# Kernel optimization log

Measured on AMD Instinct MI355X. Metric: run time of the kernel, lower is better.

## Reference

```python
import jax, jax.numpy as jnp
import numpy as np

N = 8192
E = 131072
IN_DIM = 3000
HID = 512      # gcn1 out = HID // 2 = 256
OUT = 64
EPS = 1e-12


def gcn_conv(x, W, b, src, dst, n):
    """PyG GCNConv: add self-loops, symmetric norm, gather-matmul-scatter."""
    xw = x @ W                                   # [n, out]
    loop = jnp.arange(n, dtype=src.dtype)
    s = jnp.concatenate([src, loop])             # source j
    d = jnp.concatenate([dst, loop])             # target i
    deg = jax.ops.segment_sum(jnp.ones(s.shape[0], dtype=xw.dtype), d, num_segments=n)
    dinv = deg ** -0.5                           # deg >= 1 due to self-loops
    norm = dinv[s] * dinv[d]                     # [E+n]
    out = jax.ops.segment_sum(norm[:, None] * xw[s], d, num_segments=n)
    return out + b


def avg_readout(emb, mask):
    vsum = mask @ emb                            # [N, h]
    row_sum = jnp.sum(mask, axis=1, keepdims=True)
    g = vsum / row_sum
    nrm = jnp.maximum(jnp.linalg.norm(g, axis=1, keepdims=True), EPS)
    return g / nrm                               # F.normalize(p=2, dim=1)


def bilinear(h, c, Wd, bd):
    # nn.Bilinear(n_h, n_h, 1): out[n,o] = sum_ij h[n,i] Wd[o,i,j] c[n,j] + bd[o]
    return jnp.einsum('ni,oij,nj->no', h, Wd, c) + bd


def setup_inputs() -> dict:
    key = jax.random.key(0)
    k1, k2, k3, k4, k5, k6, k7 = jax.random.split(key, 7)
    gene_data = jax.random.normal(k1, (N, IN_DIM), dtype=jnp.float32)
    # sparse binary neighborhood mask (~16 neighbors/row) + self so row sums > 0
    mask = (jax.random.uniform(k2, (N, N)) < (16.0 / N)).astype(jnp.float32)
    mask = jnp.maximum(mask, jnp.eye(N, dtype=jnp.float32))
    spatial_edge_index = jax.random.randint(k3, (2, E), 0, N, dtype=jnp.int64)
    perm = jax.random.permutation(k4, N).astype(jnp.int64)
    h1 = HID // 2
    W1 = jax.random.normal(k5, (IN_DIM, h1), dtype=jnp.float32) / np.sqrt(IN_DIM)
    b1 = jnp.zeros((h1,), dtype=jnp.float32)
    W2 = jax.random.normal(k6, (h1, OUT), dtype=jnp.float32) / np.sqrt(h1)
    b2 = jnp.zeros((OUT,), dtype=jnp.float32)
    Wd = jax.random.normal(k7, (1, OUT, OUT), dtype=jnp.float32) / np.sqrt(OUT)
    bd = jnp.zeros((1,), dtype=jnp.float32)
    return {"gene_data": gene_data, "mask": mask, "W1": W1, "b1": b1,
            "W2": W2, "b2": b2, "Wd": Wd, "bd": bd,
            "spatial_edge_index": spatial_edge_index, "perm": perm}


def reference(gene_data, mask, W1, b1, W2, b2, Wd, bd, spatial_edge_index, perm):
    src, dst = spatial_edge_index[0], spatial_edge_index[1]
    n = gene_data.shape[0]
    x1 = gene_data
    x1_c = gene_data[perm]                       # permuted (corrupted) graph
    # dropout inactive (eval mode, p=0.0)
    x1 = jax.nn.relu(gcn_conv(x1, W1, b1, src, dst, n))
    x1_c = jax.nn.relu(gcn_conv(x1_c, W1, b1, src, dst, n))
    x1 = jax.nn.relu(gcn_conv(x1, W2, b2, src, dst, n))
    x1_c = jax.nn.relu(gcn_conv(x1_c, W2, b2, src, dst, n))
    g1 = jax.nn.sigmoid(avg_readout(x1, mask))
    g1_c = jax.nn.sigmoid(avg_readout(x1_c, mask))
    ret1 = jnp.concatenate([bilinear(x1, g1, Wd, bd), bilinear(x1_c, g1, Wd, bd)], axis=1)
    ret1_c = jnp.concatenate([bilinear(x1_c, g1_c, Wd, bd), bilinear(x1, g1_c, Wd, bd)], axis=1)
    return (x1, ret1, ret1_c)
```

## Files before the change

### kernel.cpp

```cpp
#include <hip/hip_runtime.h>
#include <hip/hip_bf16.h>

#define NN 8192
#define NMASK 8191
#define IND 3000
#define H1 256
#define OUTD 64

typedef __bf16 bf16x8 __attribute__((ext_vector_type(8)));
typedef float floatx4 __attribute__((ext_vector_type(4)));

__device__ __forceinline__ unsigned short f2b(float f) {
    __hip_bfloat16 h = __float2bfloat16(f);
    unsigned short u;
    __builtin_memcpy(&u, &h, 2);
    return u;
}


__global__ void k_probe(float code, float* out) {
    if (threadIdx.x == 0 && blockIdx.x == 0) out[0] = code;
}


__global__ void k_detect64(const unsigned* __restrict__ raw, int pairs, int* __restrict__ flag) {
    __shared__ int cnt;
    if (threadIdx.x == 0) cnt = 0;
    __syncthreads();
    int z = 0;
    for (int k = threadIdx.x; k < pairs; k += blockDim.x)
        if (raw[2 * k + 1] == 0u) z++;
    atomicAdd(&cnt, z);
    __syncthreads();
    if (threadIdx.x == 0) *flag = (cnt > pairs / 2) ? 1 : 0;
}

__global__ void k_norm_idx(const unsigned* __restrict__ raw, const int* __restrict__ flag,
                           int* __restrict__ out, int count) {
    int i = blockIdx.x * blockDim.x + threadIdx.x;
    if (i < count) {
        unsigned v = (*flag) ? raw[2 * (size_t)i] : raw[i];
        out[i] = (int)(v & (unsigned)NMASK);
    }
}


__global__ void k_degree(const int* __restrict__ dst, int* __restrict__ deg, int E) {
    int e = blockIdx.x * blockDim.x + threadIdx.x;
    if (e < E) atomicAdd(&deg[dst[e]], 1);
}

__global__ __launch_bounds__(1024) void k_scan(const int* __restrict__ deg,
                                               int* __restrict__ row_ptr,
                                               int* __restrict__ cursor,
                                               float* __restrict__ dinv, int n) {
    __shared__ int sums[1024];
    int t = threadIdx.x;
    int per = n / 1024;
    int base = t * per;
    int s = 0;
    for (int u = 0; u < per; ++u) s += deg[base + u];
    sums[t] = s;
    __syncthreads();
    for (int off = 1; off < 1024; off <<= 1) {
        int v = (t >= off) ? sums[t - off] : 0;
        __syncthreads();
        sums[t] += v;
        __syncthreads();
    }
    int run = (t == 0) ? 0 : sums[t - 1];
    for (int u = 0; u < per; ++u) {
        int i = base + u;
        row_ptr[i] = run;
        cursor[i] = run;
        int d = deg[i];
        dinv[i] = rsqrtf((float)(1 + d));
        run += d;
    }
    if (t == 1023) row_ptr[n] = run;
}

__global__ void k_scatter(const int* __restrict__ src, const int* __restrict__ dst,
                          int* __restrict__ cursor, int* __restrict__ col, int E) {
    int e = blockIdx.x * blockDim.x + threadIdx.x;
    if (e < E) {
        int d = dst[e];
        int p = atomicAdd(&cursor[d], 1);
        if (p >= 0 && p < E) col[p] = src[e];
    }
}

__global__ void k_transpose_f2b(const float* __restrict__ in,
                                __hip_bfloat16* __restrict__ out, int R, int C) {
    int idx = blockIdx.x * blockDim.x + threadIdx.x;
    if (idx < R * C) {
        int r = idx / C, c = idx % C;
        out[(size_t)c * R + r] = __float2bfloat16(in[idx]);
    }
}


template <int AFP32>
__global__ __launch_bounds__(256) void k_gemm_bt(const void* __restrict__ Araw,
                                                 const __hip_bfloat16* __restrict__ Bt,
                                                 float* __restrict__ C,
                                                 int M, int N, int K) {
    __shared__ __align__(16) unsigned short As[64 * 40];
    __shared__ __align__(16) unsigned short Bs[64 * 40];
    int t = threadIdx.x;
    int m0 = blockIdx.x * 64;
    int n0 = blockIdx.y * 64;
    int lane = t & 63;
    int w = t >> 6;
    int srow = t >> 2;
    int schunk = (t & 3) * 8;
    size_t aoff = (size_t)(m0 + srow) * K + schunk;
    const unsigned short* Brow = (const unsigned short*)Bt + (size_t)(n0 + srow) * K + schunk;

    floatx4 acc0 = {0.f, 0.f, 0.f, 0.f}, acc1 = acc0, acc2 = acc0, acc3 = acc0;
    int msub = w * 16;
    int arow = msub + (lane & 15);
    int koff = (lane >> 4) * 8;
    int nlo = lane & 15;

    for (int k0 = 0; k0 < K; k0 += 32) {
        uint4 av = make_uint4(0u, 0u, 0u, 0u);
        uint4 bv = make_uint4(0u, 0u, 0u, 0u);
        if (k0 + schunk < K) {
            if (AFP32) {
                const float* ap = (const float*)Araw + aoff + k0;
                float4 f0 = *reinterpret_cast<const float4*>(ap);
                float4 f1 = *reinterpret_cast<const float4*>(ap + 4);
                unsigned short t8[8] = {f2b(f0.x), f2b(f0.y), f2b(f0.z), f2b(f0.w),
                                        f2b(f1.x), f2b(f1.y), f2b(f1.z), f2b(f1.w)};
                __builtin_memcpy(&av, t8, 16);
            } else {
                av = *reinterpret_cast<const uint4*>((const unsigned short*)Araw + aoff + k0);
            }
            bv = *reinterpret_cast<const uint4*>(Brow + k0);
        }
        __syncthreads();
        *reinterpret_cast<uint4*>(&As[srow * 40 + schunk]) = av;
        *reinterpret_cast<uint4*>(&Bs[srow * 40 + schunk]) = bv;
        __syncthreads();
        bf16x8 af = *reinterpret_cast<const bf16x8*>(&As[arow * 40 + koff]);
        bf16x8 bf0 = *reinterpret_cast<const bf16x8*>(&Bs[(0 + nlo) * 40 + koff]);
        bf16x8 bf1 = *reinterpret_cast<const bf16x8*>(&Bs[(16 + nlo) * 40 + koff]);
        bf16x8 bf2 = *reinterpret_cast<const bf16x8*>(&Bs[(32 + nlo) * 40 + koff]);
        bf16x8 bf3 = *reinterpret_cast<const bf16x8*>(&Bs[(48 + nlo) * 40 + koff]);
        acc0 = __builtin_amdgcn_mfma_f32_16x16x32_bf16(af, bf0, acc0, 0, 0, 0);
        acc1 = __builtin_amdgcn_mfma_f32_16x16x32_bf16(af, bf1, acc1, 0, 0, 0);
        acc2 = __builtin_amdgcn_mfma_f32_16x16x32_bf16(af, bf2, acc2, 0, 0, 0);
        acc3 = __builtin_amdgcn_mfma_f32_16x16x32_bf16(af, bf3, acc3, 0, 0, 0);
    }
    int crow = msub + (lane >> 4) * 4;
    int ccol = lane & 15;
    floatx4 accs[4] = {acc0, acc1, acc2, acc3};
#pragma unroll
    for (int j = 0; j < 4; ++j) {
#pragma unroll
        for (int r = 0; r < 4; ++r) {
            C[(size_t)(m0 + crow + r) * N + (n0 + j * 16 + ccol)] = accs[j][r];
        }
    }
}


__global__ __launch_bounds__(256) void k_agg1(const float* __restrict__ xw1,
                                              const int* __restrict__ row_ptr,
                                              const int* __restrict__ col,
                                              const float* __restrict__ dinv,
                                              const int* __restrict__ perm,
                                              const float* __restrict__ b1,
                                              __hip_bfloat16* __restrict__ h_all, int n) {
    __shared__ int colS[64];
    __shared__ int pcolS[64];
    __shared__ float wS[64];
    int i = blockIdx.x;
    int c = threadIdx.x;
    float di = dinv[i];
    int pi = perm[i];
    float sw = di * di;
    float acc = sw * xw1[(size_t)i * H1 + c];
    float accc = sw * xw1[(size_t)pi * H1 + c];
    int s = row_ptr[i], e = row_ptr[i + 1];
    for (int base = s; base < e; base += 64) {
        int cnt = min(64, e - base);
        __syncthreads();
        if (c < cnt) {
            int j = col[base + c];
            colS[c] = j;
            wS[c] = di * dinv[j];
            pcolS[c] = perm[j];
        }
        __syncthreads();
#pragma unroll 4
        for (int u = 0; u < cnt; ++u) {
            float wv = wS[u];
            acc += wv * xw1[(size_t)colS[u] * H1 + c];
            accc += wv * xw1[(size_t)pcolS[u] * H1 + c];
        }
    }
    float b = b1[c];
    h_all[(size_t)i * H1 + c] = __float2bfloat16(fmaxf(acc + b, 0.f));
    h_all[(size_t)(n + i) * H1 + c] = __float2bfloat16(fmaxf(accc + b, 0.f));
}


__global__ __launch_bounds__(256) void k_agg2(const float* __restrict__ hw_all,
                                              const int* __restrict__ row_ptr,
                                              const int* __restrict__ col,
                                              const float* __restrict__ dinv,
                                              const float* __restrict__ b2,
                                              float* __restrict__ x1_all,
                                              float* __restrict__ out_x1, int n) {
    int lane = threadIdx.x & 63;
    int i = blockIdx.x * 4 + (threadIdx.x >> 6);
    float di = dinv[i];
    float sw = di * di;
    float acc = sw * hw_all[(size_t)i * OUTD + lane];
    float accc = sw * hw_all[(size_t)(n + i) * OUTD + lane];
    int s = row_ptr[i], e = row_ptr[i + 1];
    for (int t = s; t < e; ++t) {
        int j = col[t];
        float wv = di * dinv[j];
        acc += wv * hw_all[(size_t)j * OUTD + lane];
        accc += wv * hw_all[(size_t)(n + j) * OUTD + lane];
    }
    float b = b2[lane];
    float v = fmaxf(acc + b, 0.f);
    float vc = fmaxf(accc + b, 0.f);
    x1_all[(size_t)i * OUTD + lane] = v;
    x1_all[(size_t)(n + i) * OUTD + lane] = vc;
    out_x1[(size_t)i * OUTD + lane] = v;
}


__global__ __launch_bounds__(256) void k_readout(const float* __restrict__ mask,
                                                 const float* __restrict__ x1_all,
                                                 float* __restrict__ g_all, int n) {
    int i = blockIdx.x;
    int lane = threadIdx.x & 63;
    int w = threadIdx.x >> 6;
    float acc = 0.f, accc = 0.f, rs = 0.f;
    const float* mrow = mask + (size_t)i * n;
    int quarter = n >> 2;
    int qbase = w * quarter;
    int iters = quarter / 256;
    for (int it = 0; it < iters; ++it) {
        int jb = qbase + it * 256 + lane * 4;
        float4 q = *reinterpret_cast<const float4*>(mrow + jb);
        bool nz = (q.x != 0.f) || (q.y != 0.f) || (q.z != 0.f) || (q.w != 0.f);
        unsigned long long bal = __ballot(nz);
        while (bal) {
            int l = __builtin_ctzll(bal);
            bal &= bal - 1;
            float s0 = __shfl(q.x, l), s1 = __shfl(q.y, l);
            float s2 = __shfl(q.z, l), s3 = __shfl(q.w, l);
            int j0 = qbase + it * 256 + l * 4;
            float sv[4] = {s0, s1, s2, s3};
#pragma unroll
            for (int u = 0; u < 4; ++u) {
                if (sv[u] != 0.f) {
                    float m = sv[u];
                    int j = j0 + u;
                    acc += m * x1_all[(size_t)j * OUTD + lane];
                    accc += m * x1_all[(size_t)(n + j) * OUTD + lane];
                    rs += m;
                }
            }
        }
    }
    __shared__ float sa[4][64], sc[4][64], sr[4];
    sa[w][lane] = acc;
    sc[w][lane] = accc;
    if (lane == 0) sr[w] = rs;
    __syncthreads();
    if (w == 0) {
        float tot = sa[0][lane] + sa[1][lane] + sa[2][lane] + sa[3][lane];
        float totc = sc[0][lane] + sc[1][lane] + sc[2][lane] + sc[3][lane];
        float rst = fmaxf(sr[0] + sr[1] + sr[2] + sr[3], 1e-20f);
        float g = tot / rst;
        float gc = totc / rst;
        float s1 = g * g, s2 = gc * gc;
#pragma unroll
        for (int off = 32; off; off >>= 1) {
            s1 += __shfl_xor(s1, off);
            s2 += __shfl_xor(s2, off);
        }
        float gn = g / fmaxf(sqrtf(s1), 1e-12f);
        float gnc = gc / fmaxf(sqrtf(s2), 1e-12f);
        g_all[(size_t)i * OUTD + lane] = 1.f / (1.f + __expf(-gn));
        g_all[(size_t)(n + i) * OUTD + lane] = 1.f / (1.f + __expf(-gnc));
    }
}


__global__ __launch_bounds__(256) void k_bilinear(const float* __restrict__ x1_all,
                                                  const float* __restrict__ g_all,
                                                  const float* __restrict__ Wd,
                                                  const float* __restrict__ bd,
                                                  float* __restrict__ out_ret1,
                                                  float* __restrict__ out_ret1c, int n) {
    __shared__ float WdS[64][65];
    __shared__ float gS[4][64], gcS[4][64];
    int t = threadIdx.x;
    for (int u = t; u < 64 * 64; u += 256) WdS[u >> 6][u & 63] = Wd[u];
    int lane = t & 63;
    int q = t >> 6;
    int i = blockIdx.x * 4 + q;
    float g = g_all[(size_t)i * OUTD + lane];
    float gc = g_all[(size_t)(n + i) * OUTD + lane];
    gS[q][lane] = g;
    gcS[q][lane] = gc;
    __syncthreads();
    float tg = 0.f, tgc = 0.f;
#pragma unroll 8
    for (int j = 0; j < 64; ++j) {
        float wv = WdS[lane][j];
        tg += wv * gS[q][j];
        tgc += wv * gcS[q][j];
    }
    float x = x1_all[(size_t)i * OUTD + lane];
    float xc = x1_all[(size_t)(n + i) * OUTD + lane];
    float r0 = x * tg, r1 = xc * tg, r2 = xc * tgc, r3 = x * tgc;
#pragma unroll
    for (int off = 32; off; off >>= 1) {
        r0 += __shfl_down(r0, off);
        r1 += __shfl_down(r1, off);
        r2 += __shfl_down(r2, off);
        r3 += __shfl_down(r3, off);
    }
    if (lane == 0) {
        float b = bd[0];
        out_ret1[(size_t)i * 2 + 0] = r0 + b;
        out_ret1[(size_t)i * 2 + 1] = r1 + b;
        out_ret1c[(size_t)i * 2 + 0] = r2 + b;
        out_ret1c[(size_t)i * 2 + 1] = r3 + b;
    }
}


extern "C" void kernel_launch(void* const* d_in, const int* in_sizes, int n_in,
                              void* d_out, int out_size, void* d_ws, size_t ws_size,
                              hipStream_t stream) {
    const float* gene = (const float*)d_in[0];
    const float* mask = (const float*)d_in[1];
    const float* W1 = (const float*)d_in[2];
    const float* b1 = (const float*)d_in[3];
    const float* W2 = (const float*)d_in[4];
    const float* b2 = (const float*)d_in[5];
    const float* Wd = (const float*)d_in[6];
    const float* bd = (const float*)d_in[7];
    const unsigned* eidx_raw = (const unsigned*)d_in[8];
    const unsigned* perm_raw = (const unsigned*)d_in[9];
    const int n = NN;
    const int E = in_sizes[8] / 2;

    char* base = (char*)d_ws;
    char* p = base;
    auto alloc = [&](size_t bytes) -> char* {
        char* r = p;
        p += (bytes + 255) & ~(size_t)255;
        return r;
    };
    int* flags = (int*)alloc(256);
    int* eidx32 = (int*)alloc((size_t)2 * E * 4);
    int* perm32 = (int*)alloc((size_t)n * 4);
    int* deg = (int*)alloc((size_t)n * 4);
    int* row_ptr = (int*)alloc((size_t)(n + 1) * 4);
    int* cursor = (int*)alloc((size_t)n * 4);
    float* dinv = (float*)alloc((size_t)n * 4);
    int* col = (int*)alloc((size_t)E * 4);
    __hip_bfloat16* W2t = (__hip_bfloat16*)alloc((size_t)H1 * OUTD * 2);
    __hip_bfloat16* W1t = (__hip_bfloat16*)alloc((size_t)IND * H1 * 2);
    float* xw1 = (float*)alloc((size_t)n * H1 * 4);
    __hip_bfloat16* h_all = (__hip_bfloat16*)alloc((size_t)2 * n * H1 * 2);
    size_t need = (size_t)(p - base);
    float* hw_all = xw1;
    float* x1_all = xw1 + (size_t)2 * n * OUTD;
    float* g_all = (float*)h_all;

    float* out_x1 = (float*)d_out;
    float* out_ret1 = out_x1 + (size_t)n * OUTD;
    float* out_ret1c = out_ret1 + (size_t)n * 2;

    if (ws_size < need) {
        k_probe<<<1, 64, 0, stream>>>(1000.f + (float)(ws_size >> 20), out_x1);
        return;
    }

    hipMemsetAsync(flags, 0, 256, stream);
    hipMemsetAsync(deg, 0, (size_t)n * 4, stream);

    k_detect64<<<1, 256, 0, stream>>>(eidx_raw, 2048, &flags[0]);
    k_detect64<<<1, 256, 0, stream>>>(perm_raw, 2048, &flags[1]);
    k_norm_idx<<<(2 * E + 255) / 256, 256, 0, stream>>>(eidx_raw, &flags[0], eidx32, 2 * E);
    k_norm_idx<<<(n + 255) / 256, 256, 0, stream>>>(perm_raw, &flags[1], perm32, n);
    const int* srcv = eidx32;
    const int* dstv = eidx32 + E;

    k_degree<<<(E + 255) / 256, 256, 0, stream>>>(dstv, deg, E);
    k_scan<<<1, 1024, 0, stream>>>(deg, row_ptr, cursor, dinv, n);
    k_scatter<<<(E + 255) / 256, 256, 0, stream>>>(srcv, dstv, cursor, col, E);

    k_transpose_f2b<<<(IND * H1 + 255) / 256, 256, 0, stream>>>(W1, W1t, IND, H1);
    k_transpose_f2b<<<(H1 * OUTD + 255) / 256, 256, 0, stream>>>(W2, W2t, H1, OUTD);

    k_gemm_bt<1><<<dim3(n / 64, H1 / 64), 256, 0, stream>>>(gene, W1t, xw1, n, H1, IND);

    k_agg1<<<n, H1, 0, stream>>>(xw1, row_ptr, col, dinv, perm32, b1, h_all, n);

    k_gemm_bt<0><<<dim3(2 * n / 64, OUTD / 64), 256, 0, stream>>>(h_all, W2t, hw_all, 2 * n, OUTD, H1);

    k_agg2<<<n / 4, 256, 0, stream>>>(hw_all, row_ptr, col, dinv, b2, x1_all, out_x1, n);

    k_readout<<<n, 256, 0, stream>>>(mask, x1_all, g_all, n);

    k_bilinear<<<n / 4, 256, 0, stream>>>(x1_all, g_all, Wd, bd, out_ret1, out_ret1c, n);
}
```

Baseline: 632.8 us.

## Fuse prep kernels, widen GEMM1 K-tile, fold bilinear into readout

Merges the two detect launches into one, and folds index normalisation and degree counting into a single prep kernel. GEMM1 now takes a 64-wide K step with a padded W1t leading dimension and swaps its grid order so column blocks of the same row tile run adjacently. The bilinear score is computed inside the readout kernel using shuffles, which removes the g_all round trip and one launch. The mask is read with nontemporal loads and the agg2 loop is unrolled. The padded W1t tail is never written; the kernel relies on the k-bound checks to keep it out of the result.

```diff
diff --git a/kernel.cpp b/kernel.cpp
--- a/kernel.cpp
+++ b/kernel.cpp
@@ -4,6 +4,7 @@
 #define NN 8192
 #define NMASK 8191
 #define IND 3000
+#define INDP 3008
 #define H1 256
 #define OUTD 64
 
@@ -23,32 +24,39 @@
 }
 
 
-__global__ void k_detect64(const unsigned* __restrict__ raw, int pairs, int* __restrict__ flag) {
+__global__ void k_detect2(const unsigned* __restrict__ a, const unsigned* __restrict__ b,
+                          int pairs, int* __restrict__ flags) {
+    const unsigned* r = (blockIdx.x == 0) ? a : b;
     __shared__ int cnt;
     if (threadIdx.x == 0) cnt = 0;
     __syncthreads();
     int z = 0;
     for (int k = threadIdx.x; k < pairs; k += blockDim.x)
-        if (raw[2 * k + 1] == 0u) z++;
+        if (r[2 * k + 1] == 0u) z++;
     atomicAdd(&cnt, z);
     __syncthreads();
-    if (threadIdx.x == 0) *flag = (cnt > pairs / 2) ? 1 : 0;
-}
-
-__global__ void k_norm_idx(const unsigned* __restrict__ raw, const int* __restrict__ flag,
-                           int* __restrict__ out, int count) {
+    if (threadIdx.x == 0) flags[blockIdx.x] = (cnt > pairs / 2) ? 1 : 0;
+}
+
+
+__global__ void k_prep(const unsigned* __restrict__ eraw, const unsigned* __restrict__ praw,
+                       const int* __restrict__ flags, int* __restrict__ eidx32,
+                       int* __restrict__ perm32, int* __restrict__ deg, int E, int n) {
     int i = blockIdx.x * blockDim.x + threadIdx.x;
-    if (i < count) {
-        unsigned v = (*flag) ? raw[2 * (size_t)i] : raw[i];
-        out[i] = (int)(v & (unsigned)NMASK);
-    }
-}
-
-
-__global__ void k_degree(const int* __restrict__ dst, int* __restrict__ deg, int E) {
-    int e = blockIdx.x * blockDim.x + threadIdx.x;
-    if (e < E) atomicAdd(&deg[dst[e]], 1);
-}
+    if (i < 2 * E) {
+        unsigned v = flags[0] ? eraw[2 * (size_t)i] : eraw[i];
+        int x = (int)(v & (unsigned)NMASK);
+        eidx32[i] = x;
+        if (i >= E) atomicAdd(&deg[x], 1);
+    } else {
+        int j = i - 2 * E;
+        if (j < n) {
+            unsigned v = flags[1] ? praw[2 * (size_t)j] : praw[j];
+            perm32[j] = (int)(v & (unsigned)NMASK);
+        }
+    }
+}
+
 
 __global__ __launch_bounds__(1024) void k_scan(const int* __restrict__ deg,
                                                int* __restrict__ row_ptr,
@@ -91,20 +99,95 @@
 }
 
 __global__ void k_transpose_f2b(const float* __restrict__ in,
-                                __hip_bfloat16* __restrict__ out, int R, int C) {
+                                __hip_bfloat16* __restrict__ out, int R, int C, int ld) {
     int idx = blockIdx.x * blockDim.x + threadIdx.x;
     if (idx < R * C) {
         int r = idx / C, c = idx % C;
-        out[(size_t)c * R + r] = __float2bfloat16(in[idx]);
-    }
-}
-
-
-template <int AFP32>
-__global__ __launch_bounds__(256) void k_gemm_bt(const void* __restrict__ Araw,
-                                                 const __hip_bfloat16* __restrict__ Bt,
-                                                 float* __restrict__ C,
-                                                 int M, int N, int K) {
+        out[(size_t)c * ld + r] = __float2bfloat16(in[idx]);
+    }
+}
+
+
+__global__ __launch_bounds__(256) void k_gemm1(const float* __restrict__ A,
+                                               const __hip_bfloat16* __restrict__ Bt,
+                                               float* __restrict__ C) {
+    __shared__ __align__(16) unsigned short As[64 * 72];
+    __shared__ __align__(16) unsigned short Bs[64 * 72];
+    int t = threadIdx.x;
+    int n0 = blockIdx.x * 64;
+    int m0 = blockIdx.y * 64;
+    int lane = t & 63;
+    int w = t >> 6;
+    int srow = t >> 2;
+    int schunk = (t & 3) * 16;
+    const float* Arow = A + (size_t)(m0 + srow) * IND + schunk;
+    const unsigned short* Brow = (const unsigned short*)Bt + (size_t)(n0 + srow) * INDP + schunk;
+
+    floatx4 acc0 = {0.f, 0.f, 0.f, 0.f}, acc1 = acc0, acc2 = acc0, acc3 = acc0;
+    int msub = w * 16;
+    int arow = msub + (lane & 15);
+    int koff = (lane >> 4) * 8;
+    int nlo = lane & 15;
+
+    for (int k0 = 0; k0 < IND; k0 += 64) {
+        uint4 av0 = make_uint4(0u, 0u, 0u, 0u), av1 = av0, bv0 = av0, bv1 = av0;
+        {
+            int kk = k0 + schunk;
+            if (kk < IND) {
+                const float* ap = Arow + k0;
+                float4 f0 = *reinterpret_cast<const float4*>(ap);
+                float4 f1 = *reinterpret_cast<const float4*>(ap + 4);
+                unsigned short t8[8] = {f2b(f0.x), f2b(f0.y), f2b(f0.z), f2b(f0.w),
+                                        f2b(f1.x), f2b(f1.y), f2b(f1.z), f2b(f1.w)};
+                __builtin_memcpy(&av0, t8, 16);
+                bv0 = *reinterpret_cast<const uint4*>(Brow + k0);
+            }
+            if (kk + 8 < IND) {
+                const float* ap = Arow + k0 + 8;
+                float4 f0 = *reinterpret_cast<const float4*>(ap);
+                float4 f1 = *reinterpret_cast<const float4*>(ap + 4);
+                unsigned short t8[8] = {f2b(f0.x), f2b(f0.y), f2b(f0.z), f2b(f0.w),
+                                        f2b(f1.x), f2b(f1.y), f2b(f1.z), f2b(f1.w)};
+                __builtin_memcpy(&av1, t8, 16);
+                bv1 = *reinterpret_cast<const uint4*>(Brow + k0 + 8);
+            }
+        }
+        __syncthreads();
+        *reinterpret_cast<uint4*>(&As[srow * 72 + schunk]) = av0;
+        *reinterpret_cast<uint4*>(&As[srow * 72 + schunk + 8]) = av1;
+        *reinterpret_cast<uint4*>(&Bs[srow * 72 + schunk]) = bv0;
+        *reinterpret_cast<uint4*>(&Bs[srow * 72 + schunk + 8]) = bv1;
+        __syncthreads();
+#pragma unroll
+        for (int ks = 0; ks < 64; ks += 32) {
+            bf16x8 af = *reinterpret_cast<const bf16x8*>(&As[arow * 72 + ks + koff]);
+            bf16x8 b0 = *reinterpret_cast<const bf16x8*>(&Bs[(0 + nlo) * 72 + ks + koff]);
+            bf16x8 b1 = *reinterpret_cast<const bf16x8*>(&Bs[(16 + nlo) * 72 + ks + koff]);
+            bf16x8 b2 = *reinterpret_cast<const bf16x8*>(&Bs[(32 + nlo) * 72 + ks + koff]);
+            bf16x8 b3 = *reinterpret_cast<const bf16x8*>(&Bs[(48 + nlo) * 72 + ks + koff]);
+            acc0 = __builtin_amdgcn_mfma_f32_16x16x32_bf16(af, b0, acc0, 0, 0, 0);
+            acc1 = __builtin_amdgcn_mfma_f32_16x16x32_bf16(af, b1, acc1, 0, 0, 0);
+            acc2 = __builtin_amdgcn_mfma_f32_16x16x32_bf16(af, b2, acc2, 0, 0, 0);
+            acc3 = __builtin_amdgcn_mfma_f32_16x16x32_bf16(af, b3, acc3, 0, 0, 0);
+        }
+    }
+    int crow = msub + (lane >> 4) * 4;
+    int ccol = lane & 15;
+    floatx4 accs[4] = {acc0, acc1, acc2, acc3};
+#pragma unroll
+    for (int j = 0; j < 4; ++j) {
+#pragma unroll
+        for (int r = 0; r < 4; ++r) {
+            C[(size_t)(m0 + crow + r) * H1 + (n0 + j * 16 + ccol)] = accs[j][r];
+        }
+    }
+}
+
+
+__global__ __launch_bounds__(256) void k_gemm2(const __hip_bfloat16* __restrict__ A,
+                                               const __hip_bfloat16* __restrict__ Bt,
+                                               float* __restrict__ C,
+                                               int M, int N, int K) {
     __shared__ __align__(16) unsigned short As[64 * 40];
     __shared__ __align__(16) unsigned short Bs[64 * 40];
     int t = threadIdx.x;
@@ -124,21 +207,8 @@
     int nlo = lane & 15;
 
     for (int k0 = 0; k0 < K; k0 += 32) {
-        uint4 av = make_uint4(0u, 0u, 0u, 0u);
-        uint4 bv = make_uint4(0u, 0u, 0u, 0u);
-        if (k0 + schunk < K) {
-            if (AFP32) {
-                const float* ap = (const float*)Araw + aoff + k0;
-                float4 f0 = *reinterpret_cast<const float4*>(ap);
-                float4 f1 = *reinterpret_cast<const float4*>(ap + 4);
-                unsigned short t8[8] = {f2b(f0.x), f2b(f0.y), f2b(f0.z), f2b(f0.w),
-                                        f2b(f1.x), f2b(f1.y), f2b(f1.z), f2b(f1.w)};
-                __builtin_memcpy(&av, t8, 16);
-            } else {
-                av = *reinterpret_cast<const uint4*>((const unsigned short*)Araw + aoff + k0);
-            }
-            bv = *reinterpret_cast<const uint4*>(Brow + k0);
-        }
+        uint4 av = *reinterpret_cast<const uint4*>((const unsigned short*)A + aoff + k0);
+        uint4 bv = *reinterpret_cast<const uint4*>(Brow + k0);
         __syncthreads();
         *reinterpret_cast<uint4*>(&As[srow * 40 + schunk]) = av;
         *reinterpret_cast<uint4*>(&Bs[srow * 40 + schunk]) = bv;
@@ -221,6 +291,7 @@
     float acc = sw * hw_all[(size_t)i * OUTD + lane];
     float accc = sw * hw_all[(size_t)(n + i) * OUTD + lane];
     int s = row_ptr[i], e = row_ptr[i + 1];
+#pragma unroll 4
     for (int t = s; t < e; ++t) {
         int j = col[t];
         float wv = di * dinv[j];
@@ -238,7 +309,10 @@
 
 __global__ __launch_bounds__(256) void k_readout(const float* __restrict__ mask,
                                                  const float* __restrict__ x1_all,
-                                                 float* __restrict__ g_all, int n) {
+                                                 const float* __restrict__ Wd,
+                                                 const float* __restrict__ bd,
+                                                 float* __restrict__ ret1,
+                                                 float* __restrict__ ret1c, int n) {
     int i = blockIdx.x;
     int lane = threadIdx.x & 63;
     int w = threadIdx.x >> 6;
@@ -249,14 +323,14 @@
     int iters = quarter / 256;
     for (int it = 0; it < iters; ++it) {
         int jb = qbase + it * 256 + lane * 4;
-        float4 q = *reinterpret_cast<const float4*>(mrow + jb);
-        bool nz = (q.x != 0.f) || (q.y != 0.f) || (q.z != 0.f) || (q.w != 0.f);
+        floatx4 q = __builtin_nontemporal_load(reinterpret_cast<const floatx4*>(mrow + jb));
+        bool nz = (q[0] != 0.f) || (q[1] != 0.f) || (q[2] != 0.f) || (q[3] != 0.f);
         unsigned long long bal = __ballot(nz);
         while (bal) {
             int l = __builtin_ctzll(bal);
             bal &= bal - 1;
-            float s0 = __shfl(q.x, l), s1 = __shfl(q.y, l);
-            float s2 = __shfl(q.z, l), s3 = __shfl(q.w, l);
+            float s0 = __shfl(q[0], l), s1 = __shfl(q[1], l);
+            float s2 = __shfl(q[2], l), s3 = __shfl(q[3], l);
             int j0 = qbase + it * 256 + l * 4;
             float sv[4] = {s0, s1, s2, s3};
 #pragma unroll
@@ -290,53 +364,35 @@
         }
         float gn = g / fmaxf(sqrtf(s1), 1e-12f);
         float gnc = gc / fmaxf(sqrtf(s2), 1e-12f);
-        g_all[(size_t)i * OUTD + lane] = 1.f / (1.f + __expf(-gn));
-        g_all[(size_t)(n + i) * OUTD + lane] = 1.f / (1.f + __expf(-gnc));
-    }
-}
-
-
-__global__ __launch_bounds__(256) void k_bilinear(const float* __restrict__ x1_all,
-                                                  const float* __restrict__ g_all,
-                                                  const float* __restrict__ Wd,
-                                                  const float* __restrict__ bd,
-                                                  float* __restrict__ out_ret1,
-                                                  float* __restrict__ out_ret1c, int n) {
-    __shared__ float WdS[64][65];
-    __shared__ float gS[4][64], gcS[4][64];
-    int t = threadIdx.x;
-    for (int u = t; u < 64 * 64; u += 256) WdS[u >> 6][u & 63] = Wd[u];
-    int lane = t & 63;
-    int q = t >> 6;
-    int i = blockIdx.x * 4 + q;
-    float g = g_all[(size_t)i * OUTD + lane];
-    float gc = g_all[(size_t)(n + i) * OUTD + lane];
-    gS[q][lane] = g;
-    gcS[q][lane] = gc;
-    __syncthreads();
-    float tg = 0.f, tgc = 0.f;
+        float gsig = 1.f / (1.f + __expf(-gn));
+        float gcsig = 1.f / (1.f + __expf(-gnc));
+        float tg = 0.f, tgc = 0.f;
+        const float* wrow = Wd + lane * 64;
 #pragma unroll 8
-    for (int j = 0; j < 64; ++j) {
-        float wv = WdS[lane][j];
-        tg += wv * gS[q][j];
-        tgc += wv * gcS[q][j];
-    }
-    float x = x1_all[(size_t)i * OUTD + lane];
-    float xc = x1_all[(size_t)(n + i) * OUTD + lane];
-    float r0 = x * tg, r1 = xc * tg, r2 = xc * tgc, r3 = x * tgc;
-#pragma unroll
-    for (int off = 32; off; off >>= 1) {
-        r0 += __shfl_down(r0, off);
-        r1 += __shfl_down(r1, off);
-        r2 += __shfl_down(r2, off);
-        r3 += __shfl_down(r3, off);
-    }
-    if (lane == 0) {
-        float b = bd[0];
-        out_ret1[(size_t)i * 2 + 0] = r0 + b;
-        out_ret1[(size_t)i * 2 + 1] = r1 + b;
-        out_ret1c[(size_t)i * 2 + 0] = r2 + b;
-        out_ret1c[(size_t)i * 2 + 1] = r3 + b;
+        for (int j = 0; j < 64; ++j) {
+            float gj = __shfl(gsig, j);
+            float gcj = __shfl(gcsig, j);
+            float wv = wrow[j];
+            tg += wv * gj;
+            tgc += wv * gcj;
+        }
+        float x = x1_all[(size_t)i * OUTD + lane];
+        float xc = x1_all[(size_t)(n + i) * OUTD + lane];
+        float r0 = x * tg, r1 = xc * tg, r2 = xc * tgc, r3 = x * tgc;
+#pragma unroll
+        for (int off = 32; off; off >>= 1) {
+            r0 += __shfl_down(r0, off);
+            r1 += __shfl_down(r1, off);
+            r2 += __shfl_down(r2, off);
+            r3 += __shfl_down(r3, off);
+        }
+        if (lane == 0) {
+            float b = bd[0];
+            ret1[(size_t)i * 2 + 0] = r0 + b;
+            ret1[(size_t)i * 2 + 1] = r1 + b;
+            ret1c[(size_t)i * 2 + 0] = r2 + b;
+            ret1c[(size_t)i * 2 + 1] = r3 + b;
+        }
     }
 }
 
@@ -373,13 +429,12 @@
     float* dinv = (float*)alloc((size_t)n * 4);
     int* col = (int*)alloc((size_t)E * 4);
     __hip_bfloat16* W2t = (__hip_bfloat16*)alloc((size_t)H1 * OUTD * 2);
-    __hip_bfloat16* W1t = (__hip_bfloat16*)alloc((size_t)IND * H1 * 2);
+    __hip_bfloat16* W1t = (__hip_bfloat16*)alloc((size_t)INDP * H1 * 2);
     float* xw1 = (float*)alloc((size_t)n * H1 * 4);
     __hip_bfloat16* h_all = (__hip_bfloat16*)alloc((size_t)2 * n * H1 * 2);
     size_t need = (size_t)(p - base);
     float* hw_all = xw1;
     float* x1_all = xw1 + (size_t)2 * n * OUTD;
-    float* g_all = (float*)h_all;
 
     float* out_x1 = (float*)d_out;
     float* out_ret1 = out_x1 + (size_t)n * OUTD;
@@ -390,32 +445,27 @@
         return;
     }
 
-    hipMemsetAsync(flags, 0, 256, stream);
     hipMemsetAsync(deg, 0, (size_t)n * 4, stream);
 
-    k_detect64<<<1, 256, 0, stream>>>(eidx_raw, 2048, &flags[0]);
-    k_detect64<<<1, 256, 0, stream>>>(perm_raw, 2048, &flags[1]);
-    k_norm_idx<<<(2 * E + 255) / 256, 256, 0, stream>>>(eidx_raw, &flags[0], eidx32, 2 * E);
-    k_norm_idx<<<(n + 255) / 256, 256, 0, stream>>>(perm_raw, &flags[1], perm32, n);
+    k_detect2<<<2, 256, 0, stream>>>(eidx_raw, perm_raw, 2048, flags);
+    k_prep<<<(2 * E + n + 255) / 256, 256, 0, stream>>>(eidx_raw, perm_raw, flags,
+                                                        eidx32, perm32, deg, E, n);
     const int* srcv = eidx32;
     const int* dstv = eidx32 + E;
 
-    k_degree<<<(E + 255) / 256, 256, 0, stream>>>(dstv, deg, E);
     k_scan<<<1, 1024, 0, stream>>>(deg, row_ptr, cursor, dinv, n);
     k_scatter<<<(E + 255) / 256, 256, 0, stream>>>(srcv, dstv, cursor, col, E);
 
-    k_transpose_f2b<<<(IND * H1 + 255) / 256, 256, 0, stream>>>(W1, W1t, IND, H1);
-    k_transpose_f2b<<<(H1 * OUTD + 255) / 256, 256, 0, stream>>>(W2, W2t, H1, OUTD);
-
-    k_gemm_bt<1><<<dim3(n / 64, H1 / 64), 256, 0, stream>>>(gene, W1t, xw1, n, H1, IND);
+    k_transpose_f2b<<<(IND * H1 + 255) / 256, 256, 0, stream>>>(W1, W1t, IND, H1, INDP);
+    k_transpose_f2b<<<(H1 * OUTD + 255) / 256, 256, 0, stream>>>(W2, W2t, H1, OUTD, H1);
+
+    k_gemm1<<<dim3(H1 / 64, n / 64), 256, 0, stream>>>(gene, W1t, xw1);
 
     k_agg1<<<n, H1, 0, stream>>>(xw1, row_ptr, col, dinv, perm32, b1, h_all, n);
 
-    k_gemm_bt<0><<<dim3(2 * n / 64, OUTD / 64), 256, 0, stream>>>(h_all, W2t, hw_all, 2 * n, OUTD, H1);
+    k_gemm2<<<dim3(2 * n / 64, OUTD / 64), 256, 0, stream>>>(h_all, W2t, hw_all, 2 * n, OUTD, H1);
 
     k_agg2<<<n / 4, 256, 0, stream>>>(hw_all, row_ptr, col, dinv, b2, x1_all, out_x1, n);
 
-    k_readout<<<n, 256, 0, stream>>>(mask, x1_all, g_all, n);
-
-    k_bilinear<<<n / 4, 256, 0, stream>>>(x1_all, g_all, Wd, bd, out_ret1, out_ret1c, n);
-}
+    k_readout<<<n, 256, 0, stream>>>(mask, x1_all, Wd, bd, out_ret1, out_ret1c, n);
+}
```

Result: faster. 606.2 us (-4.2%).
